# Kernel optimization log

Measured on AMD Instinct MI355X. Metric: run time of the kernel, lower is better.

Reference implementation:

```python
import jax, jax.numpy as jnp
import numpy as np

FEATURE_DIM = 256
LN_EPS = 1e-5        # torch nn.LayerNorm default
WHITEN_EPS = 1e-4    # whitening_eps init arg


def setup_inputs() -> dict:
    key = jax.random.key(0)
    k1, _ = jax.random.split(key)
    B, T, D = 64, 2048, FEATURE_DIM
    x = jax.random.normal(k1, (B, T, D), dtype=jnp.float32)
    gamma = jnp.ones((D,), dtype=jnp.float32)
    beta = jnp.zeros((D,), dtype=jnp.float32)
    return {"x": x, "gamma": gamma, "beta": beta}


def reference(x, gamma, beta):
    # x: (B, T, D)
    B, T, D = x.shape
    # LayerNorm over last dim
    mean = jnp.mean(x, axis=-1, keepdims=True)
    var = jnp.mean((x - mean) ** 2, axis=-1, keepdims=True)
    xn = (x - mean) * jax.lax.rsqrt(var + LN_EPS) * gamma + beta
    # Batched cross-frame covariance whitening (T >= 2 here)
    mu = jnp.mean(xn, axis=1, keepdims=True)          # (B, 1, D)
    xc = xn - mu                                       # (B, T, D)
    cov = jnp.einsum('btd,bte->bde', xc, xc) / (T - 1) # (B, D, D)
    cov = cov + WHITEN_EPS * jnp.eye(D, dtype=x.dtype)
    eigvals, eigvecs = jnp.linalg.eigh(cov)            # (B, D), (B, D, D)
    inv_sqrt_vals = jax.lax.rsqrt(jnp.clip(eigvals, WHITEN_EPS, None))  # (B, D)
    # inv_sqrt = V diag(w^-1/2) V^T
    inv_sqrt = jnp.einsum('bde,be,bfe->bdf', eigvecs, inv_sqrt_vals, eigvecs)
    out = jnp.einsum('btd,bdf->btf', xc, inv_sqrt)
    return out
```

## Files before the change

kernel.cpp:

```cpp
#include <hip/hip_runtime.h>
#include <cstddef>

#define TT 2048
#define BB 64
#define DD 256
#define LN_EPS 1e-5f
#define WEPS 1e-4f

typedef __attribute__((ext_vector_type(8))) short short8;
typedef __attribute__((ext_vector_type(4))) float f32x4;
typedef __attribute__((ext_vector_type(8))) _Float16 f16x8;
typedef __attribute__((ext_vector_type(4))) _Float16 f16x4;

__device__ __forceinline__ unsigned short f2h(float f) {
  _Float16 h = (_Float16)f;
  return *(unsigned short*)&h;
}
__device__ __forceinline__ float h2f(unsigned short u) {
  _Float16 h = *(_Float16*)&u;
  return (float)h;
}
__device__ __forceinline__ void gload16(unsigned short* lds, const unsigned short* g) {
  __builtin_amdgcn_global_load_lds(
      (const __attribute__((address_space(1))) void*)g,
      (__attribute__((address_space(3))) void*)lds, 16, 0, 0);
}

__global__ __launch_bounds__(256) void prepass_kernel(const float* __restrict__ x,
    float* __restrict__ stats, float* __restrict__ part) {
  int c = blockIdx.x;
  int b = blockIdx.y;
  int tid = threadIdx.x;
  int wave = tid >> 6, lane = tid & 63;
  int rowbase = b * TT + c * 128 + wave * 32;
  const float* xb = x + (size_t)rowbase * DD + lane * 4;
  float a0 = 0.f, a1 = 0.f, a2 = 0.f, a3 = 0.f;
  for (int i = 0; i < 32; ++i) {
    float4 v = *(const float4*)&xb[(size_t)i * DD];
    float s  = v.x + v.y + v.z + v.w;
    float sq = v.x*v.x + v.y*v.y + v.z*v.z + v.w*v.w;
    #pragma unroll
    for (int off = 32; off; off >>= 1) { s += __shfl_xor(s, off); sq += __shfl_xor(sq, off); }
    float mean = s * (1.f/DD);
    float var  = fmaxf(sq * (1.f/DD) - mean*mean, 0.f);
    float rstd = rsqrtf(var + LN_EPS);
    if (lane == 0) {
      stats[2*(rowbase+i)]   = mean;
      stats[2*(rowbase+i)+1] = rstd;
    }
    a0 += (v.x - mean) * rstd;
    a1 += (v.y - mean) * rstd;
    a2 += (v.z - mean) * rstd;
    a3 += (v.w - mean) * rstd;
  }
  int pidx = c * 4 + wave;
  *(float4*)&part[((size_t)pidx*BB + b)*DD + lane*4] = make_float4(a0, a1, a2, a3);
}

__global__ __launch_bounds__(256) void mu_finalize_kernel(const float* __restrict__ part,
                                                          const float* __restrict__ gamma,
                                                          const float* __restrict__ beta,
                                                          float* __restrict__ mu) {
  int b = blockIdx.x;
  int d = threadIdx.x;
  float s = 0.f;
  #pragma unroll 8
  for (int c = 0; c < 64; ++c) s += part[((size_t)c*BB + b)*DD + d];
  mu[b*DD + d] = gamma[d] * s * (1.f/TT) + beta[d];
}

__global__ __launch_bounds__(256) void cov_mfma(const float* __restrict__ x,
    const float* __restrict__ stats, const float* __restrict__ gamma,
    const float* __restrict__ beta, const float* __restrict__ mu,
    unsigned short* __restrict__ Ch) {
  int flat = blockIdx.y * gridDim.x + blockIdx.x;
  int kx = flat & 7, j = flat >> 3;
  int b = (kx << 3) + j / 10;
  int tile = j - (j / 10) * 10;
  int p = 0, t = tile;
  while (t >= 4 - p) { t -= (4 - p); ++p; }
  int q = p + t;
  int i0 = p * 64, j0 = q * 64;
  bool diag = (p == q);

  __shared__ unsigned short sm[16384];
  __shared__ float sGi[64], sBi[64], sGj[64], sBj[64];

  int tid = threadIdx.x;
  const float* mub = mu + (size_t)b*DD;
  if (tid < 64) {
    sGi[tid] = gamma[i0+tid]; sBi[tid] = beta[i0+tid] - mub[i0+tid];
    sGj[tid] = gamma[j0+tid]; sBj[tid] = beta[j0+tid] - mub[j0+tid];
  }
  __syncthreads();

  int wave = tid >> 6, lane = tid & 63;
  int lr = lane & 15, lg = lane >> 4;
  int tg4 = tid >> 4;
  int dg  = tid & 15;
  int d0 = dg * 4;
  const float* xb  = x + (size_t)b*TT*DD;
  const float* stb = stats + (size_t)b*TT*2;

  float4 gi4 = *(const float4*)&sGi[d0];
  float4 bi4 = *(const float4*)&sBi[d0];
  float4 gj4 = *(const float4*)&sGj[d0];
  float4 bj4 = *(const float4*)&sBj[d0];

  int ch16 = tg4 >> 1, half = tg4 & 1;
  int widx[4];
  #pragma unroll
  for (int jj = 0; jj < 4; ++jj) {
    int dl = d0 + jj;
    int swz = (ch16 ^ (dl & 7) ^ ((dl >> 3) & 7)) & 7;
    widx[jj] = dl*64 + swz*8 + half*4;
  }

  f32x4 acc[4] = {};

  #define COV_STAGE(k0v, dst)                                                  \
  {                                                                            \
    int trow = (k0v) + tg4 * 4;                                                \
    float4 s01 = *(const float4*)&stb[2*trow];                                 \
    float4 s23 = *(const float4*)&stb[2*trow + 4];                             \
    float mm[4] = {s01.x, s01.z, s23.x, s23.z};                                \
    float rr[4] = {s01.y, s01.w, s23.y, s23.w};                                \
    {                                                                          \
      _Float16 va[4][4];                                                       \
      _Pragma("unroll")                                                        \
      for (int i = 0; i < 4; ++i) {                                            \
        float4 v = *(const float4*)&xb[(size_t)(trow+i)*DD + i0 + d0];         \
        va[i][0] = (_Float16)(((v.x - mm[i]) * rr[i]) * gi4.x + bi4.x);        \
        va[i][1] = (_Float16)(((v.y - mm[i]) * rr[i]) * gi4.y + bi4.y);        \
        va[i][2] = (_Float16)(((v.z - mm[i]) * rr[i]) * gi4.z + bi4.z);        \
        va[i][3] = (_Float16)(((v.w - mm[i]) * rr[i]) * gi4.w + bi4.w);        \
      }                                                                        \
      _Pragma("unroll")                                                        \
      for (int jj = 0; jj < 4; ++jj) {                                         \
        f16x4 w = {va[0][jj], va[1][jj], va[2][jj], va[3][jj]};                \
        *(f16x4*)&(dst)[widx[jj]] = w;                                         \
      }                                                                        \
    }                                                                          \
    if (!diag) {                                                               \
      _Float16 vb[4][4];                                                       \
      _Pragma("unroll")                                                        \
      for (int i = 0; i < 4; ++i) {                                            \
        float4 v = *(const float4*)&xb[(size_t)(trow+i)*DD + j0 + d0];         \
        vb[i][0] = (_Float16)(((v.x - mm[i]) * rr[i]) * gj4.x + bj4.x);        \
        vb[i][1] = (_Float16)(((v.y - mm[i]) * rr[i]) * gj4.y + bj4.y);        \
        vb[i][2] = (_Float16)(((v.z - mm[i]) * rr[i]) * gj4.z + bj4.z);        \
        vb[i][3] = (_Float16)(((v.w - mm[i]) * rr[i]) * gj4.w + bj4.w);        \
      }                                                                        \
      _Pragma("unroll")                                                        \
      for (int jj = 0; jj < 4; ++jj) {                                         \
        f16x4 w = {vb[0][jj], vb[1][jj], vb[2][jj], vb[3][jj]};                \
        *(f16x4*)&(dst)[4096 + widx[jj]] = w;                                  \
      }                                                                        \
    }                                                                          \
  }

  COV_STAGE(0, sm);
  __syncthreads();

  for (int kk = 0; kk < 32; ++kk) {
    unsigned short* cur = sm + (kk & 1) * 8192;
    if (kk < 31) {
      unsigned short* nxt = sm + ((kk & 1) ^ 1) * 8192;
      COV_STAGE((kk + 1) * 64, nxt);
    }
    const unsigned short* pA = cur;
    const unsigned short* pB = diag ? cur : (cur + 4096);
    #pragma unroll
    for (int ks = 0; ks < 2; ++ks) {
      int rowA = wave*16 + lr;
      int cc = ks*4 + lg;
      int aoff = rowA*64 + (((cc ^ (rowA&7) ^ ((rowA>>3)&7)) & 7) << 3);
      f16x8 av = *(const f16x8*)&pA[aoff];
      #pragma unroll
      for (int n = 0; n < 4; ++n) {
        int rowB = n*16 + lr;
        int boff = rowB*64 + (((cc ^ (rowB&7) ^ ((rowB>>3)&7)) & 7) << 3);
        f16x8 bv = *(const f16x8*)&pB[boff];
        acc[n] = __builtin_amdgcn_mfma_f32_16x16x32_f16(av, bv, acc[n], 0, 0, 0);
      }
    }
    __syncthreads();
  }
  #undef COV_STAGE

  float* sC = (float*)sm;
  #pragma unroll
  for (int n = 0; n < 4; ++n)
    #pragma unroll
    for (int r = 0; r < 4; ++r)
      sC[(wave*16 + lg*4 + r)*65 + n*16 + lr] = acc[n][r];
  __syncthreads();
  unsigned short* Chb = Ch + (size_t)b*DD*DD;
  const float invTm1 = 1.f / (float)(TT - 1);
  int row = tid >> 2, cb = (tid & 3) * 16;
  int gi = i0 + row;
  unsigned short hv[16];
  #pragma unroll
  for (int e = 0; e < 16; ++e) {
    float v = sC[row*65 + cb + e] * invTm1;
    int gj = j0 + cb + e;
    if (gi == gj) v += WEPS;
    hv[e] = f2h(v);
    if (!diag) Chb[(size_t)gj*DD + gi] = hv[e];
  }
  size_t go = (size_t)gi*DD + j0 + cb;
  *(short8*)&Chb[go]     = *(short8*)&hv[0];
  *(short8*)&Chb[go + 8] = *(short8*)&hv[8];
}

__global__ __launch_bounds__(256) void power_kernel(
    const unsigned short* __restrict__ Ch, float* __restrict__ sbuf) {
  int b = blockIdx.x, tid = threadIdx.x;
  __shared__ unsigned short sC[DD*DD];
  __shared__ float v[DD];
  __shared__ float red[4];
  const unsigned short* Cb = Ch + (size_t)b*DD*DD;
  #pragma unroll
  for (int i = 0; i < 32; ++i) {
    int chunkid = i*256 + tid;
    int r = chunkid >> 5, ch = chunkid & 31;
    short8 qv = *(const short8*)&Cb[(size_t)chunkid*8];
    *(short8*)&sC[r*256 + ((ch ^ (r & 7)) << 3)] = qv;
  }
  unsigned u = (unsigned)tid * 2654435761u;
  v[tid] = 0.5f + (float)((u >> 9) & 1023) * (1.f/1024.f);
  __syncthreads();
  float lam = 1.f;
  for (int it = 0; it < 10; ++it) {
    float w = 0.f;
    #pragma unroll
    for (int ch = 0; ch < 32; ++ch) {
      short8 hq = *(const short8*)&sC[tid*256 + ((ch ^ (tid & 7)) << 3)];
      const float* vp = &v[ch*8];
      #pragma unroll
      for (int e = 0; e < 8; ++e) w += h2f((unsigned short)hq[e]) * vp[e];
    }
    float ssq = w * w;
    #pragma unroll
    for (int off = 32; off; off >>= 1) ssq += __shfl_xor(ssq, off);
    if ((tid & 63) == 0) red[tid >> 6] = ssq;
    __syncthreads();
    float nrm = sqrtf(red[0] + red[1] + red[2] + red[3]);
    lam = nrm;
    v[tid] = w / nrm;
    __syncthreads();
  }
  if (tid == 0) sbuf[b] = lam * 1.05f;
}

__device__ __forceinline__ void bgemm_tile2(
    const unsigned short* __restrict__ A, const unsigned short* __restrict__ B,
    unsigned short* __restrict__ C,
    float alpha, float diagBeta, int tilex, int b, unsigned short* sm) {
  const int tid = threadIdx.x;
  const int i0g = (tilex >> 1) * 128, j0g = (tilex & 1) * 128;
  const size_t mb = (size_t)b * DD * DD;
  const int wave = tid >> 6, lane = tid & 63;
  const int wr = wave >> 2, wc = wave & 3;
  const int lr = lane & 15, lg = lane >> 4;

  f32x4 acc[8] = {};

  #pragma unroll
  for (int p2 = 0; p2 < 2; ++p2) {
    int slot = tid + p2 * 512;
    int row = slot >> 3, c = slot & 7;
    int srcc = (c ^ (row & 7)) << 3;
    int base = (wave * 64 + p2 * 512) * 8;
    gload16(&sm[base], A + mb + (size_t)(i0g + row) * DD + srcc);
    gload16(&sm[8192 + base], B + mb + (size_t)(j0g + row) * DD + srcc);
  }
  __syncthreads();

  #pragma unroll
  for (int kk = 0; kk < 4; ++kk) {
    unsigned short* cur = sm + (kk & 1) * 16384;
    if (kk < 3) {
      unsigned short* nxt = sm + ((kk & 1) ^ 1) * 16384;
      int k0n = (kk + 1) * 64;
      #pragma unroll
      for (int p2 = 0; p2 < 2; ++p2) {
        int slot = tid + p2 * 512;
        int row = slot >> 3, c = slot & 7;
        int srcc = (c ^ (row & 7)) << 3;
        int base = (wave * 64 + p2 * 512) * 8;
        gload16(&nxt[base], A + mb + (size_t)(i0g + row) * DD + k0n + srcc);
        gload16(&nxt[8192 + base], B + mb + (size_t)(j0g + row) * DD + k0n + srcc);
      }
    }
    #pragma unroll
    for (int ks = 0; ks < 2; ++ks) {
      int cc = ks * 4 + lg;
      f16x8 bv[2];
      #pragma unroll
      for (int n = 0; n < 2; ++n) {
        int rowB = wc * 32 + n * 16 + lr;
        int boff = rowB * 64 + ((cc ^ (rowB & 7)) * 8);
        bv[n] = *(const f16x8*)&cur[8192 + boff];
      }
      #pragma unroll
      for (int m = 0; m < 4; ++m) {
        int rowA = wr * 64 + m * 16 + lr;
        int aoff = rowA * 64 + ((cc ^ (rowA & 7)) * 8);
        f16x8 av = *(const f16x8*)&cur[aoff];
        #pragma unroll
        for (int n = 0; n < 2; ++n)
          acc[m*2+n] = __builtin_amdgcn_mfma_f32_16x16x32_f16(av, bv[n], acc[m*2+n], 0, 0, 0);
      }
    }
    __syncthreads();
  }

  #pragma unroll
  for (int m = 0; m < 4; ++m) {
    #pragma unroll
    for (int n = 0; n < 2; ++n) {
      int col = j0g + wc * 32 + n * 16 + lr;
      int row0 = i0g + wr * 64 + m * 16 + lg * 4;
      #pragma unroll
      for (int r = 0; r < 4; ++r) {
        float vv = alpha * acc[m*2+n][r];
        int row = row0 + r;
        if (row == col) vv += diagBeta;
        C[mb + (size_t)row * DD + col] = f2h(vv);
      }
    }
  }
}

__global__ __launch_bounds__(512) void bgemm_mfma2(
    const unsigned short* __restrict__ A, const unsigned short* __restrict__ B,
    unsigned short* __restrict__ C, float alpha, float diagBeta) {
  __shared__ unsigned short sm[32768];
  int flat = blockIdx.y * gridDim.x + blockIdx.x;
  int kx = flat & 7, j = flat >> 3;
  int b = (kx << 3) + (j >> 2);
  int tile = j & 3;
  bgemm_tile2(A, B, C, alpha, diagBeta, tile, b, sm);
}

__global__ __launch_bounds__(512) void bgemm_dual2(
    const unsigned short* __restrict__ A0, const unsigned short* __restrict__ B0,
    unsigned short* __restrict__ C0,
    const unsigned short* __restrict__ A1, const unsigned short* __restrict__ B1,
    unsigned short* __restrict__ C1) {
  __shared__ unsigned short sm[32768];
  int flat = blockIdx.y * gridDim.x + blockIdx.x;
  int kx = flat & 7, j = flat >> 3;
  int b = (kx << 3) + (j >> 3);
  int t8 = j & 7;
  int half = t8 >> 2, tile = t8 & 3;
  if (half == 0)
    bgemm_tile2(A0, B0, C0, 0.5f, 0.f, tile, b, sm);
  else
    bgemm_tile2(A1, B1, C1, 0.5f, 0.f, tile, b, sm);
}

__global__ __launch_bounds__(512) void bgemm_p0(
    const unsigned short* __restrict__ C, unsigned short* __restrict__ Y1,
    unsigned short* __restrict__ Z1, const float* __restrict__ sbuf) {
  __shared__ unsigned short sm[32768];
  int flat = blockIdx.y * gridDim.x + blockIdx.x;
  int kx = flat & 7, j = flat >> 3;
  int b = (kx << 3) + (j >> 2);
  int tilex = j & 3;

  const int tid = threadIdx.x;
  const int i0g = (tilex >> 1) * 128, j0g = (tilex & 1) * 128;
  const size_t mb = (size_t)b * DD * DD;
  const int wave = tid >> 6, lane = tid & 63;
  const int wr = wave >> 2, wc = wave & 3;
  const int lr = lane & 15, lg = lane >> 4;

  f32x4 acc[8] = {};

  #pragma unroll
  for (int p2 = 0; p2 < 2; ++p2) {
    int slot = tid + p2 * 512;
    int row = slot >> 3, c = slot & 7;
    int srcc = (c ^ (row & 7)) << 3;
    int base = (wave * 64 + p2 * 512) * 8;
    gload16(&sm[base], C + mb + (size_t)(i0g + row) * DD + srcc);
    gload16(&sm[8192 + base], C + mb + (size_t)(j0g + row) * DD + srcc);
  }
  __syncthreads();

  #pragma unroll
  for (int kk = 0; kk < 4; ++kk) {
    unsigned short* cur = sm + (kk & 1) * 16384;
    if (kk < 3) {
      unsigned short* nxt = sm + ((kk & 1) ^ 1) * 16384;
      int k0n = (kk + 1) * 64;
      #pragma unroll
      for (int p2 = 0; p2 < 2; ++p2) {
        int slot = tid + p2 * 512;
        int row = slot >> 3, c = slot & 7;
        int srcc = (c ^ (row & 7)) << 3;
        int base = (wave * 64 + p2 * 512) * 8;
        gload16(&nxt[base], C + mb + (size_t)(i0g + row) * DD + k0n + srcc);
        gload16(&nxt[8192 + base], C + mb + (size_t)(j0g + row) * DD + k0n + srcc);
      }
    }
    #pragma unroll
    for (int ks = 0; ks < 2; ++ks) {
      int cc = ks * 4 + lg;
      f16x8 bv[2];
      #pragma unroll
      for (int n = 0; n < 2; ++n) {
        int rowB = wc * 32 + n * 16 + lr;
        int boff = rowB * 64 + ((cc ^ (rowB & 7)) * 8);
        bv[n] = *(const f16x8*)&cur[8192 + boff];
      }
      #pragma unroll
      for (int m = 0; m < 4; ++m) {
        int rowA = wr * 64 + m * 16 + lr;
        int aoff = rowA * 64 + ((cc ^ (rowA & 7)) * 8);
        f16x8 av = *(const f16x8*)&cur[aoff];
        #pragma unroll
        for (int n = 0; n < 2; ++n)
          acc[m*2+n] = __builtin_amdgcn_mfma_f32_16x16x32_f16(av, bv[n], acc[m*2+n], 0, 0, 0);
      }
    }
    __syncthreads();
  }

  float invs = 1.f / sbuf[b];
  float a2 = -0.5f * invs * invs;
  float a1c = 1.5f * invs;
  float z1c = -0.5f * invs;
  #pragma unroll
  for (int m = 0; m < 4; ++m) {
    #pragma unroll
    for (int n = 0; n < 2; ++n) {
      int col = j0g + wc * 32 + n * 16 + lr;
      int row0 = i0g + wr * 64 + m * 16 + lg * 4;
      #pragma unroll
      for (int r = 0; r < 4; ++r) {
        int row = row0 + r;
        float cv = h2f(C[mb + (size_t)row * DD + col]);
        float yv = a2 * acc[m*2+n][r] + a1c * cv;
        float zv = z1c * cv + ((row == col) ? 1.5f : 0.f);
        Y1[mb + (size_t)row * DD + col] = f2h(yv);
        Z1[mb + (size_t)row * DD + col] = f2h(zv);
      }
    }
  }
}

__global__ __launch_bounds__(512) void out_mfma2(const float* __restrict__ x,
    const float* __restrict__ stats, const float* __restrict__ gamma,
    const float* __restrict__ beta, const float* __restrict__ mu,
    const unsigned short* __restrict__ Z, const float* __restrict__ sbuf,
    float* __restrict__ out) {
  int flat = blockIdx.y * gridDim.x + blockIdx.x;
  int kx = flat & 7, j = flat >> 3;
  int b = (kx << 3) + (j >> 5);
  int tile = j & 31;
  int t0 = (tile >> 1) * 128, f0 = (tile & 1) * 128;
  __shared__ unsigned short sm[32768];
  __shared__ float sG[256], sBs[256];

  int tid = threadIdx.x;
  if (tid < 256) {
    sG[tid] = gamma[tid];
    sBs[tid] = beta[tid] - mu[(size_t)b*DD + tid];
  }
  __syncthreads();

  const int wave = tid >> 6, lane = tid & 63;
  const int wr = wave >> 2, wc = wave & 3;
  const int lr = lane & 15, lg = lane >> 4;
  const float* xb  = x + (size_t)b*TT*DD;
  const float* stb = stats + (size_t)b*TT*2;
  const unsigned short* Zb = Z + (size_t)b*DD*DD;

  f32x4 acc[8] = {};

  #define OUT_STAGE(k0v, dst)                                                  \
  {                                                                            \
    _Pragma("unroll")                                                          \
    for (int p2 = 0; p2 < 2; ++p2) {                                           \
      int slot = tid + p2 * 512;                                               \
      int row = slot >> 3, c0 = slot & 7;                                      \
      int srcc = (c0 ^ (row & 7)) << 3;                                        \
      size_t gz = (size_t)(f0 + row) * DD + (k0v) + srcc;                      \
      int base = (wave * 64 + p2 * 512) * 8;                                   \
      gload16(&(dst)[8192 + base], Zb + gz);                                   \
      int trow = t0 + row;                                                     \
      float mean = stb[2*trow], rstd = stb[2*trow+1];                          \
      const float* xr = xb + (size_t)trow*DD + (k0v) + c0*8;                   \
      _Float16 h8[8];                                                          \
      _Pragma("unroll")                                                        \
      for (int qq = 0; qq < 2; ++qq) {                                         \
        float4 v = *(const float4*)&xr[qq*4];                                  \
        float vvv[4] = {v.x, v.y, v.z, v.w};                                   \
        _Pragma("unroll")                                                      \
        for (int e2 = 0; e2 < 4; ++e2) {                                       \
          int d = (k0v) + c0*8 + qq*4 + e2;                                    \
          h8[qq*4+e2] = (_Float16)((vvv[e2] - mean) * rstd * sG[d] + sBs[d]);  \
        }                                                                      \
      }                                                                        \
      int ld = row * 64 + ((c0 ^ (row & 7)) * 8);                              \
      *(f16x8*)&(dst)[ld] = *(f16x8*)&h8[0];                                   \
    }                                                                          \
  }

  OUT_STAGE(0, sm);
  __syncthreads();

  #pragma unroll
  for (int kk = 0; kk < 4; ++kk) {
    unsigned short* cur = sm + (kk & 1) * 16384;
    if (kk < 3) {
      unsigned short* nxt = sm + ((kk & 1) ^ 1) * 16384;
      OUT_STAGE((kk + 1) * 64, nxt);
    }
    #pragma unroll
    for (int ks = 0; ks < 2; ++ks) {
      int cc = ks * 4 + lg;
      f16x8 bv[2];
      #pragma unroll
      for (int n = 0; n < 2; ++n) {
        int rowB = wc * 32 + n * 16 + lr;
        int boff = rowB * 64 + ((cc ^ (rowB & 7)) * 8);
        bv[n] = *(const f16x8*)&cur[8192 + boff];
      }
      #pragma unroll
      for (int m = 0; m < 4; ++m) {
        int rowA = wr * 64 + m * 16 + lr;
        int aoff = rowA * 64 + ((cc ^ (rowA & 7)) * 8);
        f16x8 av = *(const f16x8*)&cur[aoff];
        #pragma unroll
        for (int n = 0; n < 2; ++n)
          acc[m*2+n] = __builtin_amdgcn_mfma_f32_16x16x32_f16(av, bv[n], acc[m*2+n], 0, 0, 0);
      }
    }
    __syncthreads();
  }
  #undef OUT_STAGE

  float rs = rsqrtf(sbuf[b]);
  float* ob = out + (size_t)b*TT*DD;
  #pragma unroll
  for (int m = 0; m < 4; ++m) {
    #pragma unroll
    for (int n = 0; n < 2; ++n) {
      int col = f0 + wc * 32 + n * 16 + lr;
      int row0 = t0 + wr * 64 + m * 16 + lg * 4;
      #pragma unroll
      for (int r = 0; r < 4; ++r)
        ob[(size_t)(row0 + r)*DD + col] = acc[m*2+n][r] * rs;
    }
  }
}

extern "C" void kernel_launch(void* const* d_in, const int* in_sizes, int n_in,
                              void* d_out, int out_size, void* d_ws, size_t ws_size,
                              hipStream_t stream) {
  const float* x     = (const float*)d_in[0];
  const float* gamma = (const float*)d_in[1];
  const float* beta  = (const float*)d_in[2];
  float* out = (float*)d_out;

  float* wsf   = (float*)d_ws;
  float* stats = wsf;
  float* mu    = wsf + 262144;
  float* sbuf  = wsf + 278528;
  unsigned short* nsb = (unsigned short*)(wsf + 278784);
  const size_t MATU = (size_t)BB * DD * DD;
  unsigned short* H[5];
  for (int k = 0; k < 5; ++k) H[k] = nsb + (size_t)k * MATU;
  float* part = (float*)H[1];

  prepass_kernel<<<dim3(16, BB), 256, 0, stream>>>(x, stats, part);
  mu_finalize_kernel<<<BB, 256, 0, stream>>>(part, gamma, beta, mu);
  cov_mfma<<<dim3(10, BB), 256, 0, stream>>>(x, stats, gamma, beta, mu, H[0]);
  power_kernel<<<BB, 256, 0, stream>>>(H[0], sbuf);

  bgemm_p0<<<dim3(4, BB), 512, 0, stream>>>(H[0], H[3], H[1], sbuf);
  bgemm_mfma2<<<dim3(4, BB), 512, 0, stream>>>(H[1], H[3], H[2], -1.f, 3.f);
  bgemm_dual2<<<dim3(8, BB), 512, 0, stream>>>(H[3], H[2], H[0], H[2], H[1], H[4]);
  bgemm_mfma2<<<dim3(4, BB), 512, 0, stream>>>(H[4], H[0], H[2], -1.f, 3.f);
  bgemm_dual2<<<dim3(8, BB), 512, 0, stream>>>(H[0], H[2], H[3], H[2], H[4], H[1]);
  bgemm_mfma2<<<dim3(4, BB), 512, 0, stream>>>(H[1], H[3], H[2], -1.f, 3.f);
  bgemm_mfma2<<<dim3(4, BB), 512, 0, stream>>>(H[2], H[1], H[4], 0.5f, 0.f);

  out_mfma2<<<dim3(32, BB), 512, 0, stream>>>(x, stats, gamma, beta, mu, H[4], sbuf, out);
}
```

Before: 220.2 us.

## Materialize fp16 normalized activations once and fold mean subtraction algebraically

The prepass now writes the LayerNorm output as an fp16 matrix, so the covariance and output GEMMs load it directly (the output GEMM via async global-to-LDS loads) instead of recomputing normalization from fp32 x. The mean is subtracted algebraically: the covariance subtracts T·mu·muᵀ in the epilogue, and the output subtracts a per-batch mu·W vector computed by a new small matvec kernel. The Newton-Schulz inverse-sqrt iteration is also changed to use different coefficients and one fewer iteration pair. This trades an extra fp16 activation write and read for less fp32 traffic and fewer GEMM launches. It risks accuracy loss from cancellation in the mean correction and from the shortened iteration.

New measurement: 199.8 us. 1.1x faster.

```diff
diff --git a/kernel.cpp b/kernel.cpp
--- a/kernel.cpp
+++ b/kernel.cpp
@@ -27,13 +27,17 @@
 }
 
 __global__ __launch_bounds__(256) void prepass_kernel(const float* __restrict__ x,
-    float* __restrict__ stats, float* __restrict__ part) {
+    const float* __restrict__ gamma, const float* __restrict__ beta,
+    unsigned short* __restrict__ A, float* __restrict__ part) {
   int c = blockIdx.x;
   int b = blockIdx.y;
   int tid = threadIdx.x;
   int wave = tid >> 6, lane = tid & 63;
   int rowbase = b * TT + c * 128 + wave * 32;
   const float* xb = x + (size_t)rowbase * DD + lane * 4;
+  unsigned short* Ab = A + (size_t)rowbase * DD + lane * 4;
+  float4 g4 = *(const float4*)&gamma[lane * 4];
+  float4 b4 = *(const float4*)&beta[lane * 4];
   float a0 = 0.f, a1 = 0.f, a2 = 0.f, a3 = 0.f;
   for (int i = 0; i < 32; ++i) {
     float4 v = *(const float4*)&xb[(size_t)i * DD];
@@ -44,14 +48,15 @@
     float mean = s * (1.f/DD);
     float var  = fmaxf(sq * (1.f/DD) - mean*mean, 0.f);
     float rstd = rsqrtf(var + LN_EPS);
-    if (lane == 0) {
-      stats[2*(rowbase+i)]   = mean;
-      stats[2*(rowbase+i)+1] = rstd;
-    }
-    a0 += (v.x - mean) * rstd;
-    a1 += (v.y - mean) * rstd;
-    a2 += (v.z - mean) * rstd;
-    a3 += (v.w - mean) * rstd;
+    float c0 = (v.x - mean) * rstd, c1 = (v.y - mean) * rstd;
+    float c2 = (v.z - mean) * rstd, c3 = (v.w - mean) * rstd;
+    a0 += c0; a1 += c1; a2 += c2; a3 += c3;
+    ushort4 w;
+    w.x = f2h(c0 * g4.x + b4.x);
+    w.y = f2h(c1 * g4.y + b4.y);
+    w.z = f2h(c2 * g4.z + b4.z);
+    w.w = f2h(c3 * g4.w + b4.w);
+    *(ushort4*)&Ab[(size_t)i * DD] = w;
   }
   int pidx = c * 4 + wave;
   *(float4*)&part[((size_t)pidx*BB + b)*DD + lane*4] = make_float4(a0, a1, a2, a3);
@@ -69,10 +74,8 @@
   mu[b*DD + d] = gamma[d] * s * (1.f/TT) + beta[d];
 }
 
-__global__ __launch_bounds__(256) void cov_mfma(const float* __restrict__ x,
-    const float* __restrict__ stats, const float* __restrict__ gamma,
-    const float* __restrict__ beta, const float* __restrict__ mu,
-    unsigned short* __restrict__ Ch) {
+__global__ __launch_bounds__(256) void cov_mfma(const unsigned short* __restrict__ A,
+    const float* __restrict__ mu, unsigned short* __restrict__ Ch) {
   int flat = blockIdx.y * gridDim.x + blockIdx.x;
   int kx = flat & 7, j = flat >> 3;
   int b = (kx << 3) + j / 10;
@@ -84,14 +87,11 @@
   bool diag = (p == q);
 
   __shared__ unsigned short sm[16384];
-  __shared__ float sGi[64], sBi[64], sGj[64], sBj[64];
+  __shared__ float sMu[128];
 
   int tid = threadIdx.x;
   const float* mub = mu + (size_t)b*DD;
-  if (tid < 64) {
-    sGi[tid] = gamma[i0+tid]; sBi[tid] = beta[i0+tid] - mub[i0+tid];
-    sGj[tid] = gamma[j0+tid]; sBj[tid] = beta[j0+tid] - mub[j0+tid];
-  }
+  if (tid < 64) { sMu[tid] = mub[i0+tid]; sMu[64+tid] = mub[j0+tid]; }
   __syncthreads();
 
   int wave = tid >> 6, lane = tid & 63;
@@ -99,13 +99,7 @@
   int tg4 = tid >> 4;
   int dg  = tid & 15;
   int d0 = dg * 4;
-  const float* xb  = x + (size_t)b*TT*DD;
-  const float* stb = stats + (size_t)b*TT*2;
-
-  float4 gi4 = *(const float4*)&sGi[d0];
-  float4 bi4 = *(const float4*)&sBi[d0];
-  float4 gj4 = *(const float4*)&sGj[d0];
-  float4 bj4 = *(const float4*)&sBj[d0];
+  const unsigned short* Ab = A + (size_t)b*TT*DD;
 
   int ch16 = tg4 >> 1, half = tg4 & 1;
   int widx[4];
@@ -121,41 +115,23 @@
   #define COV_STAGE(k0v, dst)                                                  \
   {                                                                            \
     int trow = (k0v) + tg4 * 4;                                                \
-    float4 s01 = *(const float4*)&stb[2*trow];                                 \
-    float4 s23 = *(const float4*)&stb[2*trow + 4];                             \
-    float mm[4] = {s01.x, s01.z, s23.x, s23.z};                                \
-    float rr[4] = {s01.y, s01.w, s23.y, s23.w};                                \
-    {                                                                          \
-      _Float16 va[4][4];                                                       \
-      _Pragma("unroll")                                                        \
-      for (int i = 0; i < 4; ++i) {                                            \
-        float4 v = *(const float4*)&xb[(size_t)(trow+i)*DD + i0 + d0];         \
-        va[i][0] = (_Float16)(((v.x - mm[i]) * rr[i]) * gi4.x + bi4.x);        \
-        va[i][1] = (_Float16)(((v.y - mm[i]) * rr[i]) * gi4.y + bi4.y);        \
-        va[i][2] = (_Float16)(((v.z - mm[i]) * rr[i]) * gi4.z + bi4.z);        \
-        va[i][3] = (_Float16)(((v.w - mm[i]) * rr[i]) * gi4.w + bi4.w);        \
-      }                                                                        \
-      _Pragma("unroll")                                                        \
-      for (int jj = 0; jj < 4; ++jj) {                                         \
-        f16x4 w = {va[0][jj], va[1][jj], va[2][jj], va[3][jj]};                \
-        *(f16x4*)&(dst)[widx[jj]] = w;                                         \
-      }                                                                        \
-    }                                                                          \
+    ushort4 sv0 = *(const ushort4*)&Ab[(size_t)(trow+0)*DD + i0 + d0];         \
+    ushort4 sv1 = *(const ushort4*)&Ab[(size_t)(trow+1)*DD + i0 + d0];         \
+    ushort4 sv2 = *(const ushort4*)&Ab[(size_t)(trow+2)*DD + i0 + d0];         \
+    ushort4 sv3 = *(const ushort4*)&Ab[(size_t)(trow+3)*DD + i0 + d0];         \
+    { ushort4 w = {sv0.x, sv1.x, sv2.x, sv3.x}; *(ushort4*)&(dst)[widx[0]] = w; } \
+    { ushort4 w = {sv0.y, sv1.y, sv2.y, sv3.y}; *(ushort4*)&(dst)[widx[1]] = w; } \
+    { ushort4 w = {sv0.z, sv1.z, sv2.z, sv3.z}; *(ushort4*)&(dst)[widx[2]] = w; } \
+    { ushort4 w = {sv0.w, sv1.w, sv2.w, sv3.w}; *(ushort4*)&(dst)[widx[3]] = w; } \
     if (!diag) {                                                               \
-      _Float16 vb[4][4];                                                       \
-      _Pragma("unroll")                                                        \
-      for (int i = 0; i < 4; ++i) {                                            \
-        float4 v = *(const float4*)&xb[(size_t)(trow+i)*DD + j0 + d0];         \
-        vb[i][0] = (_Float16)(((v.x - mm[i]) * rr[i]) * gj4.x + bj4.x);        \
-        vb[i][1] = (_Float16)(((v.y - mm[i]) * rr[i]) * gj4.y + bj4.y);        \
-        vb[i][2] = (_Float16)(((v.z - mm[i]) * rr[i]) * gj4.z + bj4.z);        \
-        vb[i][3] = (_Float16)(((v.w - mm[i]) * rr[i]) * gj4.w + bj4.w);        \
-      }                                                                        \
-      _Pragma("unroll")                                                        \
-      for (int jj = 0; jj < 4; ++jj) {                                         \
-        f16x4 w = {vb[0][jj], vb[1][jj], vb[2][jj], vb[3][jj]};                \
-        *(f16x4*)&(dst)[4096 + widx[jj]] = w;                                  \
-      }                                                                        \
+      ushort4 t0v = *(const ushort4*)&Ab[(size_t)(trow+0)*DD + j0 + d0];       \
+      ushort4 t1v = *(const ushort4*)&Ab[(size_t)(trow+1)*DD + j0 + d0];       \
+      ushort4 t2v = *(const ushort4*)&Ab[(size_t)(trow+2)*DD + j0 + d0];       \
+      ushort4 t3v = *(const ushort4*)&Ab[(size_t)(trow+3)*DD + j0 + d0];       \
+      { ushort4 w = {t0v.x, t1v.x, t2v.x, t3v.x}; *(ushort4*)&(dst)[4096 + widx[0]] = w; } \
+      { ushort4 w = {t0v.y, t1v.y, t2v.y, t3v.y}; *(ushort4*)&(dst)[4096 + widx[1]] = w; } \
+      { ushort4 w = {t0v.z, t1v.z, t2v.z, t3v.z}; *(ushort4*)&(dst)[4096 + widx[2]] = w; } \
+      { ushort4 w = {t0v.w, t1v.w, t2v.w, t3v.w}; *(ushort4*)&(dst)[4096 + widx[3]] = w; } \
     }                                                                          \
   }
 
@@ -199,11 +175,12 @@
   const float invTm1 = 1.f / (float)(TT - 1);
   int row = tid >> 2, cb = (tid & 3) * 16;
   int gi = i0 + row;
+  float mi = sMu[row] * (float)TT;
   unsigned short hv[16];
   #pragma unroll
   for (int e = 0; e < 16; ++e) {
-    float v = sC[row*65 + cb + e] * invTm1;
     int gj = j0 + cb + e;
+    float v = (sC[row*65 + cb + e] - mi * sMu[64 + cb + e]) * invTm1;
     if (gi == gj) v += WEPS;
     hv[e] = f2h(v);
     if (!diag) Chb[(size_t)gj*DD + gi] = hv[e];
@@ -430,9 +407,9 @@
   }
 
   float invs = 1.f / sbuf[b];
-  float a2 = -0.5f * invs * invs;
-  float a1c = 1.5f * invs;
-  float z1c = -0.5f * invs;
+  float a2 = -invs * invs;
+  float a1c = 2.f * invs;
+  float z1c = -invs;
   #pragma unroll
   for (int m = 0; m < 4; ++m) {
     #pragma unroll
@@ -444,7 +421,7 @@
         int row = row0 + r;
         float cv = h2f(C[mb + (size_t)row * DD + col]);
         float yv = a2 * acc[m*2+n][r] + a1c * cv;
-        float zv = z1c * cv + ((row == col) ? 1.5f : 0.f);
+        float zv = z1c * cv + ((row == col) ? 2.f : 0.f);
         Y1[mb + (size_t)row * DD + col] = f2h(yv);
         Z1[mb + (size_t)row * DD + col] = f2h(zv);
       }
@@ -452,65 +429,47 @@
   }
 }
 
-__global__ __launch_bounds__(512) void out_mfma2(const float* __restrict__ x,
-    const float* __restrict__ stats, const float* __restrict__ gamma,
-    const float* __restrict__ beta, const float* __restrict__ mu,
-    const unsigned short* __restrict__ Z, const float* __restrict__ sbuf,
-    float* __restrict__ out) {
+__global__ __launch_bounds__(256) void matvec_r(const float* __restrict__ mu,
+    const unsigned short* __restrict__ W, float* __restrict__ rvec) {
+  int b = blockIdx.x, f = threadIdx.x;
+  __shared__ float sMu[DD];
+  sMu[f] = mu[(size_t)b*DD + f];
+  __syncthreads();
+  const unsigned short* Wb = W + (size_t)b*DD*DD;
+  float acc = 0.f;
+  #pragma unroll 8
+  for (int d = 0; d < DD; ++d) acc += sMu[d] * h2f(Wb[(size_t)d*DD + f]);
+  rvec[(size_t)b*DD + f] = acc;
+}
+
+__global__ __launch_bounds__(512) void out_mfma2(const unsigned short* __restrict__ A,
+    const unsigned short* __restrict__ W, const float* __restrict__ rvec,
+    const float* __restrict__ sbuf, float* __restrict__ out) {
   int flat = blockIdx.y * gridDim.x + blockIdx.x;
   int kx = flat & 7, j = flat >> 3;
   int b = (kx << 3) + (j >> 5);
   int tile = j & 31;
   int t0 = (tile >> 1) * 128, f0 = (tile & 1) * 128;
   __shared__ unsigned short sm[32768];
-  __shared__ float sG[256], sBs[256];
 
   int tid = threadIdx.x;
-  if (tid < 256) {
-    sG[tid] = gamma[tid];
-    sBs[tid] = beta[tid] - mu[(size_t)b*DD + tid];
-  }
-  __syncthreads();
-
   const int wave = tid >> 6, lane = tid & 63;
   const int wr = wave >> 2, wc = wave & 3;
   const int lr = lane & 15, lg = lane >> 4;
-  const float* xb  = x + (size_t)b*TT*DD;
-  const float* stb = stats + (size_t)b*TT*2;
-  const unsigned short* Zb = Z + (size_t)b*DD*DD;
+  const unsigned short* Ab = A + (size_t)b*TT*DD;
+  const unsigned short* Wb = W + (size_t)b*DD*DD;
 
   f32x4 acc[8] = {};
 
-  #define OUT_STAGE(k0v, dst)                                                  \
-  {                                                                            \
-    _Pragma("unroll")                                                          \
-    for (int p2 = 0; p2 < 2; ++p2) {                                           \
-      int slot = tid + p2 * 512;                                               \
-      int row = slot >> 3, c0 = slot & 7;                                      \
-      int srcc = (c0 ^ (row & 7)) << 3;                                        \
-      size_t gz = (size_t)(f0 + row) * DD + (k0v) + srcc;                      \
-      int base = (wave * 64 + p2 * 512) * 8;                                   \
-      gload16(&(dst)[8192 + base], Zb + gz);                                   \
-      int trow = t0 + row;                                                     \
-      float mean = stb[2*trow], rstd = stb[2*trow+1];                          \
-      const float* xr = xb + (size_t)trow*DD + (k0v) + c0*8;                   \
-      _Float16 h8[8];                                                          \
-      _Pragma("unroll")                                                        \
-      for (int qq = 0; qq < 2; ++qq) {                                         \
-        float4 v = *(const float4*)&xr[qq*4];                                  \
-        float vvv[4] = {v.x, v.y, v.z, v.w};                                   \
-        _Pragma("unroll")                                                      \
-        for (int e2 = 0; e2 < 4; ++e2) {                                       \
-          int d = (k0v) + c0*8 + qq*4 + e2;                                    \
-          h8[qq*4+e2] = (_Float16)((vvv[e2] - mean) * rstd * sG[d] + sBs[d]);  \
-        }                                                                      \
-      }                                                                        \
-      int ld = row * 64 + ((c0 ^ (row & 7)) * 8);                              \
-      *(f16x8*)&(dst)[ld] = *(f16x8*)&h8[0];                                   \
-    }                                                                          \
-  }
-
-  OUT_STAGE(0, sm);
+  #pragma unroll
+  for (int p2 = 0; p2 < 2; ++p2) {
+    int slot = tid + p2 * 512;
+    int row = slot >> 3, c = slot & 7;
+    int srcc = (c ^ (row & 7)) << 3;
+    int base = (wave * 64 + p2 * 512) * 8;
+    gload16(&sm[base], Ab + (size_t)(t0 + row) * DD + srcc);
+    gload16(&sm[8192 + base], Wb + (size_t)(f0 + row) * DD + srcc);
+  }
   __syncthreads();
 
   #pragma unroll
@@ -518,7 +477,16 @@
     unsigned short* cur = sm + (kk & 1) * 16384;
     if (kk < 3) {
       unsigned short* nxt = sm + ((kk & 1) ^ 1) * 16384;
-      OUT_STAGE((kk + 1) * 64, nxt);
+      int k0n = (kk + 1) * 64;
+      #pragma unroll
+      for (int p2 = 0; p2 < 2; ++p2) {
+        int slot = tid + p2 * 512;
+        int row = slot >> 3, c = slot & 7;
+        int srcc = (c ^ (row & 7)) << 3;
+        int base = (wave * 64 + p2 * 512) * 8;
+        gload16(&nxt[base], Ab + (size_t)(t0 + row) * DD + k0n + srcc);
+        gload16(&nxt[8192 + base], Wb + (size_t)(f0 + row) * DD + k0n + srcc);
+      }
     }
     #pragma unroll
     for (int ks = 0; ks < 2; ++ks) {
@@ -542,9 +510,12 @@
     }
     __syncthreads();
   }
-  #undef OUT_STAGE
 
   float rs = rsqrtf(sbuf[b]);
+  float rv[2];
+  #pragma unroll
+  for (int n = 0; n < 2; ++n)
+    rv[n] = rvec[(size_t)b*DD + f0 + wc*32 + n*16 + lr];
   float* ob = out + (size_t)b*TT*DD;
   #pragma unroll
   for (int m = 0; m < 4; ++m) {
@@ -554,7 +525,7 @@
       int row0 = t0 + wr * 64 + m * 16 + lg * 4;
       #pragma unroll
       for (int r = 0; r < 4; ++r)
-        ob[(size_t)(row0 + r)*DD + col] = acc[m*2+n][r] * rs;
+        ob[(size_t)(row0 + r)*DD + col] = (acc[m*2+n][r] - rv[n]) * rs;
     }
   }
 }
@@ -567,28 +538,29 @@
   const float* beta  = (const float*)d_in[2];
   float* out = (float*)d_out;
 
-  float* wsf   = (float*)d_ws;
-  float* stats = wsf;
-  float* mu    = wsf + 262144;
-  float* sbuf  = wsf + 278528;
-  unsigned short* nsb = (unsigned short*)(wsf + 278784);
+  float* wsf  = (float*)d_ws;
+  float* mu   = wsf;
+  float* sbuf = wsf + 16384;
+  float* rvec = wsf + 16448;
+  unsigned short* nsb = (unsigned short*)(wsf + 32832);
   const size_t MATU = (size_t)BB * DD * DD;
   unsigned short* H[5];
   for (int k = 0; k < 5; ++k) H[k] = nsb + (size_t)k * MATU;
+  unsigned short* A = nsb + 5 * MATU;
   float* part = (float*)H[1];
 
-  prepass_kernel<<<dim3(16, BB), 256, 0, stream>>>(x, stats, part);
+  prepass_kernel<<<dim3(16, BB), 256, 0, stream>>>(x, gamma, beta, A, part);
   mu_finalize_kernel<<<BB, 256, 0, stream>>>(part, gamma, beta, mu);
-  cov_mfma<<<dim3(10, BB), 256, 0, stream>>>(x, stats, gamma, beta, mu, H[0]);
+  cov_mfma<<<dim3(10, BB), 256, 0, stream>>>(A, mu, H[0]);
   power_kernel<<<BB, 256, 0, stream>>>(H[0], sbuf);
 
   bgemm_p0<<<dim3(4, BB), 512, 0, stream>>>(H[0], H[3], H[1], sbuf);
   bgemm_mfma2<<<dim3(4, BB), 512, 0, stream>>>(H[1], H[3], H[2], -1.f, 3.f);
-  bgemm_dual2<<<dim3(8, BB), 512, 0, stream>>>(H[3], H[2], H[0], H[2], H[1], H[4]);
+  bgemm_dual2<<<dim3(8, BB), 512, 0, stream>>>(H[3], H[2], H[0],
+                                               H[2], H[1], H[4]);
   bgemm_mfma2<<<dim3(4, BB), 512, 0, stream>>>(H[4], H[0], H[2], -1.f, 3.f);
-  bgemm_dual2<<<dim3(8, BB), 512, 0, stream>>>(H[0], H[2], H[3], H[2], H[4], H[1]);
-  bgemm_mfma2<<<dim3(4, BB), 512, 0, stream>>>(H[1], H[3], H[2], -1.f, 3.f);
-  bgemm_mfma2<<<dim3(4, BB), 512, 0, stream>>>(H[2], H[1], H[4], 0.5f, 0.f);
-
-  out_mfma2<<<dim3(32, BB), 512, 0, stream>>>(x, stats, gamma, beta, mu, H[4], sbuf, out);
-}
+  bgemm_mfma2<<<dim3(4, BB), 512, 0, stream>>>(H[2], H[4], H[1], 0.5f, 0.f);
+
+  matvec_r<<<BB, 256, 0, stream>>>(mu, H[1], rvec);
+  out_mfma2<<<dim3(32, BB), 512, 0, stream>>>(A, H[1], rvec, sbuf, out);
+}
```
